# Kernel tuning notes

Hardware: AMD Instinct MI355X
Metric: run time of the kernel (lower is better)

Reference implementation:

```python
import jax, jax.numpy as jnp
import numpy as np

EPS = 1e-6

def feature_map(x):
    # 'elu' feature map: elu(x) + 1 (positive feature map from Katharopoulos et al.)
    return jax.nn.elu(x) + 1.0

def setup_inputs() -> dict:
    key = jax.random.key(0)
    kq, kk, kv = jax.random.split(key, 3)
    B, L, H, D = 4, 2048, 16, 64
    q = jax.random.normal(kq, (B, L, H, D), dtype=jnp.float32)
    k = jax.random.normal(kk, (B, L, H, D), dtype=jnp.float32)
    v = jax.random.normal(kv, (B, L, H, D), dtype=jnp.float32)
    return {"q": q, "k": k, "v": v}

def reference(q, k, v):
    # q, k, v: [N, L, H, D]  (attention_mask=None -> causal linear attention)
    qf = feature_map(q)
    kf = feature_map(k)
    # normalizer: z[n,l,h] = sum_d qf[n,l,h,d] * cumsum_s<=l kf[n,s,h,d]
    z = jnp.einsum('nlhd,nlhd->nlh', qf, jnp.cumsum(kf, axis=1)) + EPS
    # causal_dot_product via scan over sequence with carry S[n,h,d,m]
    B, L, H, D = q.shape
    M = v.shape[-1]
    qs = jnp.moveaxis(qf, 1, 0)  # [L, N, H, D]
    ks = jnp.moveaxis(kf, 1, 0)
    vs = jnp.moveaxis(v, 1, 0)

    def step(S, qkv):
        ql, kl, vl = qkv                              # [N,H,D], [N,H,D], [N,H,M]
        S = S + jnp.einsum('nhd,nhm->nhdm', kl, vl)   # running sum of k v^T
        out = jnp.einsum('nhd,nhdm->nhm', ql, S)
        return S, out

    S0 = jnp.zeros((B, H, D, M), dtype=q.dtype)
    _, outs = jax.lax.scan(step, S0, (qs, ks, vs))    # outs: [L, N, H, M]
    v_ = jnp.moveaxis(outs, 0, 1)                     # [N, L, H, M]
    return v_ / z[..., None]
```

## Files before the change

### kernel.cpp

```cpp
#include <hip/hip_runtime.h>
#include <cstdint>

#define LL 2048
#define HH 16
#define DD 64
#define NC 32
#define LSTR 1024
#define EPSF 1e-6f
#define PAD 72

typedef __bf16 bf16x8 __attribute__((ext_vector_type(8)));
typedef float floatx4 __attribute__((ext_vector_type(4)));
typedef unsigned short ushortx8 __attribute__((ext_vector_type(8)));
typedef unsigned short ushortx4 __attribute__((ext_vector_type(4)));
typedef unsigned short ushortx2 __attribute__((ext_vector_type(2)));

static __device__ __forceinline__ float fmap(float x){ return x > 0.f ? x + 1.f : __expf(x); }
static __device__ __forceinline__ unsigned short f2bf(float f){
    unsigned u = __builtin_bit_cast(unsigned, f);
    u += 0x7fffu + ((u >> 16) & 1u);
    return (unsigned short)(u >> 16);
}
static __device__ __forceinline__ float bf2f(unsigned short s){
    unsigned u = ((unsigned)s) << 16;
    return __builtin_bit_cast(float, u);
}
static __device__ __forceinline__ bf16x8 ldf(const unsigned short* p){
    return __builtin_bit_cast(bf16x8, *(const ushortx8*)p);
}

__global__ __launch_bounds__(256) void k1(const float* __restrict__ kp, const float* __restrict__ vp,
                                          unsigned short* __restrict__ kvt, float* __restrict__ ks)
{
    __shared__ __align__(16) unsigned short kft[DD*PAD];
    __shared__ __align__(16) unsigned short vtt[DD*PAD];
    const int ci = blockIdx.x;
    const int c = ci & 31, bh = ci >> 5, b = bh >> 4, h = bh & 15;
    const int t = threadIdx.x;
    const int64_t gbase = ((int64_t)(b*LL + c*DD)*HH + h)*DD;
#pragma unroll
    for (int i = 0; i < 2; ++i) {
        int flat = t + 256*i;
        int l0 = (flat >> 4) * 2, col = (flat & 15) << 2;
        const float* gk = kp + gbase + (int64_t)l0*LSTR + col;
        const float* gv = vp + gbase + (int64_t)l0*LSTR + col;
        float4 ka = *(const float4*)(gk);
        float4 kb = *(const float4*)(gk + LSTR);
        float4 va = *(const float4*)(gv);
        float4 vb = *(const float4*)(gv + LSTR);
        float kaa[4] = {ka.x,ka.y,ka.z,ka.w}, kbb[4] = {kb.x,kb.y,kb.z,kb.w};
        float vaa[4] = {va.x,va.y,va.z,va.w}, vbb[4] = {vb.x,vb.y,vb.z,vb.w};
#pragma unroll
        for (int e = 0; e < 4; ++e) {
            *(ushortx2*)(kft + (col+e)*PAD + l0) = ushortx2{ f2bf(fmap(kaa[e])), f2bf(fmap(kbb[e])) };
            *(ushortx2*)(vtt + (col+e)*PAD + l0) = ushortx2{ f2bf(vaa[e]), f2bf(vbb[e]) };
        }
    }
    __syncthreads();
    const int w = t >> 6, lane = t & 63, quad = lane >> 4, lr = lane & 15;
    const int m0 = 16*w;
    floatx4 acc[4];
#pragma unroll
    for (int dt = 0; dt < 4; ++dt) acc[dt] = floatx4{0.f,0.f,0.f,0.f};
#pragma unroll
    for (int kk = 0; kk < 2; ++kk) {
        bf16x8 a = ldf(vtt + (m0+lr)*PAD + kk*32 + quad*8);
#pragma unroll
        for (int dt = 0; dt < 4; ++dt) {
            bf16x8 bb = ldf(kft + (dt*16+lr)*PAD + kk*32 + quad*8);
            acc[dt] = __builtin_amdgcn_mfma_f32_16x16x32_bf16(a, bb, acc[dt], 0, 0, 0);
        }
    }
    unsigned short* kvo = kvt + (int64_t)ci*4096;
#pragma unroll
    for (int dt = 0; dt < 4; ++dt)
#pragma unroll
        for (int r = 0; r < 4; ++r)
            kvo[(m0 + quad*4 + r)*DD + dt*16 + lr] = f2bf(acc[dt][r]);
    if (t < DD) {
        float s = 0.f;
#pragma unroll
        for (int j = 0; j < 8; ++j) {
            ushortx8 u = *(const ushortx8*)(kft + t*PAD + j*8);
#pragma unroll
            for (int e = 0; e < 8; ++e) s += bf2f(u[e]);
        }
        ks[(int64_t)ci*DD + t] = s;
    }
}

__global__ __launch_bounds__(256) void k2(unsigned short* __restrict__ kvt, float* __restrict__ ks)
{
    const int blk = blockIdx.x;
    const int bh = blk >> 3, part = blk & 7, t = threadIdx.x;
    unsigned short* base = kvt + (int64_t)bh*NC*4096 + (part*256 + t)*2;
    float r0 = 0.f, r1 = 0.f;
    unsigned x = *(const unsigned*)base;
    for (int c = 0; c < NC-1; ++c) {
        unsigned xn = *(const unsigned*)(base + (int64_t)(c+1)*4096);
        unsigned o = (unsigned)f2bf(r0) | ((unsigned)f2bf(r1) << 16);
        r0 += bf2f((unsigned short)(x & 0xffffu));
        r1 += bf2f((unsigned short)(x >> 16));
        *(unsigned*)(base + (int64_t)c*4096) = o;
        x = xn;
    }
    *(unsigned*)(base + (int64_t)(NC-1)*4096) = (unsigned)f2bf(r0) | ((unsigned)f2bf(r1) << 16);
    if (part == 0 && t < DD) {
        float r = 0.f;
        float* kb = ks + (int64_t)bh*NC*DD + t;
        for (int c = 0; c < NC; ++c) { float xx = kb[(int64_t)c*DD]; kb[(int64_t)c*DD] = r; r += xx; }
    }
}

__global__ __launch_bounds__(256) void k3(const float* __restrict__ qp, const float* __restrict__ kp,
                                          const float* __restrict__ vp,
                                          const unsigned short* __restrict__ kvt,
                                          const float* __restrict__ ks, float* __restrict__ outp)
{
    __shared__ __align__(16) unsigned short qf [DD*PAD];
    __shared__ __align__(16) unsigned short kfx[80*PAD];
    __shared__ __align__(16) unsigned short vtt[DD*PAD];
    __shared__ float zr[DD];
    const int ci = blockIdx.x;
    const int c = ci & 31, bh = ci >> 5, b = bh >> 4, h = bh & 15;
    const int t = threadIdx.x;
    const int64_t gbase = ((int64_t)(b*LL + c*DD)*HH + h)*DD;
    const unsigned short* kvg = kvt + (int64_t)ci*4096;
    const float* ksg = ks + (int64_t)ci*DD;
#pragma unroll
    for (int i = 0; i < 2; ++i) {
        int flat = t + 256*i;
        int l0 = (flat >> 4) * 2, col = (flat & 15) << 2;
        const float* gq = qp + gbase + (int64_t)l0*LSTR + col;
        const float* gk = kp + gbase + (int64_t)l0*LSTR + col;
        const float* gv = vp + gbase + (int64_t)l0*LSTR + col;
        float4 qa = *(const float4*)(gq);
        float4 qb = *(const float4*)(gq + LSTR);
        float4 ka = *(const float4*)(gk);
        float4 kb = *(const float4*)(gk + LSTR);
        float4 va = *(const float4*)(gv);
        float4 vb = *(const float4*)(gv + LSTR);
        *(ushortx4*)(qf + l0*PAD + col)      = ushortx4{ f2bf(fmap(qa.x)), f2bf(fmap(qa.y)), f2bf(fmap(qa.z)), f2bf(fmap(qa.w)) };
        *(ushortx4*)(qf + (l0+1)*PAD + col)  = ushortx4{ f2bf(fmap(qb.x)), f2bf(fmap(qb.y)), f2bf(fmap(qb.z)), f2bf(fmap(qb.w)) };
        *(ushortx4*)(kfx + l0*PAD + col)     = ushortx4{ f2bf(fmap(ka.x)), f2bf(fmap(ka.y)), f2bf(fmap(ka.z)), f2bf(fmap(ka.w)) };
        *(ushortx4*)(kfx + (l0+1)*PAD + col) = ushortx4{ f2bf(fmap(kb.x)), f2bf(fmap(kb.y)), f2bf(fmap(kb.z)), f2bf(fmap(kb.w)) };
        float vaa[4] = {va.x,va.y,va.z,va.w}, vbb[4] = {vb.x,vb.y,vb.z,vb.w};
#pragma unroll
        for (int e = 0; e < 4; ++e)
            *(ushortx2*)(vtt + (col+e)*PAD + l0) = ushortx2{ f2bf(vaa[e]), f2bf(vbb[e]) };
    }
    if (t < 135) *(ushortx8*)(kfx + 65*PAD + t*8) = ushortx8{0,0,0,0,0,0,0,0};
    if (t < DD)  kfx[64*PAD + t] = f2bf(ksg[t]);
    __syncthreads();

    const int w = t >> 6, lane = t & 63, quad = lane >> 4, lr = lane & 15;
    const int l0 = 16*w;
    bf16x8 aq[2];
    aq[0] = ldf(qf + (l0+lr)*PAD + quad*8);
    aq[1] = ldf(qf + (l0+lr)*PAD + 32 + quad*8);
    bf16x8 bs[2][4];
#pragma unroll
    for (int kk = 0; kk < 2; ++kk)
#pragma unroll
        for (int mt = 0; mt < 4; ++mt)
            bs[kk][mt] = ldf(kvg + (mt*16+lr)*DD + kk*32 + quad*8);

    floatx4 sc[5];
#pragma unroll
    for (int tt = 0; tt < 5; ++tt) sc[tt] = floatx4{0.f,0.f,0.f,0.f};
#pragma unroll
    for (int kk = 0; kk < 2; ++kk)
#pragma unroll
        for (int tt = 0; tt < 5; ++tt) {
            bf16x8 bb = ldf(kfx + (tt*16+lr)*PAD + kk*32 + quad*8);
            sc[tt] = __builtin_amdgcn_mfma_f32_16x16x32_bf16(aq[kk], bb, sc[tt], 0, 0, 0);
        }

    float zp[4] = {0.f,0.f,0.f,0.f};
#pragma unroll
    for (int tt = 0; tt < 4; ++tt)
#pragma unroll
        for (int r = 0; r < 4; ++r) {
            int row = l0 + quad*4 + r;
            int col = tt*16 + lr;
            float val = (col <= row) ? sc[tt][r] : 0.f;
            zp[r] += val;
            qf[row*PAD + col] = f2bf(val);
        }
#pragma unroll
    for (int r = 0; r < 4; ++r) zp[r] += (lr == 0) ? sc[4][r] : 0.f;
#pragma unroll
    for (int m = 1; m < 16; m <<= 1)
#pragma unroll
        for (int r = 0; r < 4; ++r) zp[r] += __shfl_xor(zp[r], m, 64);
    if (lr == 0)
#pragma unroll
        for (int r = 0; r < 4; ++r) zr[l0 + quad*4 + r] = 1.f / (zp[r] + EPSF);

    floatx4 oa[4];
#pragma unroll
    for (int mt = 0; mt < 4; ++mt) oa[mt] = floatx4{0.f,0.f,0.f,0.f};
#pragma unroll
    for (int kk = 0; kk < 2; ++kk) {
        bf16x8 a2 = ldf(qf + (l0+lr)*PAD + kk*32 + quad*8);
#pragma unroll
        for (int mt = 0; mt < 4; ++mt) {
            bf16x8 bv = ldf(vtt + (mt*16+lr)*PAD + kk*32 + quad*8);
            oa[mt] = __builtin_amdgcn_mfma_f32_16x16x32_bf16(a2, bv, oa[mt], 0, 0, 0);
        }
    }
#pragma unroll
    for (int kk = 0; kk < 2; ++kk)
#pragma unroll
        for (int mt = 0; mt < 4; ++mt)
            oa[mt] = __builtin_amdgcn_mfma_f32_16x16x32_bf16(aq[kk], bs[kk][mt], oa[mt], 0, 0, 0);
#pragma unroll
    for (int r = 0; r < 4; ++r) {
        int row = l0 + quad*4 + r;
        float rz = zr[row];
#pragma unroll
        for (int mt = 0; mt < 4; ++mt)
            outp[gbase + (int64_t)row*LSTR + mt*16 + lr] = oa[mt][r] * rz;
    }
}

extern "C" void kernel_launch(void* const* d_in, const int* in_sizes, int n_in,
                              void* d_out, int out_size, void* d_ws, size_t ws_size,
                              hipStream_t stream) {
    const float* q = (const float*)d_in[0];
    const float* k = (const float*)d_in[1];
    const float* v = (const float*)d_in[2];
    float* out = (float*)d_out;
    unsigned short* kvt = (unsigned short*)d_ws;
    float* ks = (float*)((char*)d_ws + (size_t)2048*4096*2);
    k1<<<2048, 256, 0, stream>>>(k, v, kvt, ks);
    k2<<<512,  256, 0, stream>>>(kvt, ks);
    k3<<<2048, 256, 0, stream>>>(q, k, v, kvt, ks, out);
}
```

Baseline: 156.0 us.

## Fuse three-kernel chunked linear attention into one sequential-scan kernel with double buffering

```diff
diff --git a/kernel.cpp b/kernel.cpp
--- a/kernel.cpp
+++ b/kernel.cpp
@@ -1,13 +1,8 @@
 #include <hip/hip_runtime.h>
 #include <cstdint>
 
-#define LL 2048
-#define HH 16
-#define DD 64
-#define NC 32
-#define LSTR 1024
 #define EPSF 1e-6f
-#define PAD 72
+#define P 72
 
 typedef __bf16 bf16x8 __attribute__((ext_vector_type(8)));
 typedef float floatx4 __attribute__((ext_vector_type(4)));
@@ -21,206 +16,155 @@
     u += 0x7fffu + ((u >> 16) & 1u);
     return (unsigned short)(u >> 16);
 }
-static __device__ __forceinline__ float bf2f(unsigned short s){
-    unsigned u = ((unsigned)s) << 16;
-    return __builtin_bit_cast(float, u);
-}
 static __device__ __forceinline__ bf16x8 ldf(const unsigned short* p){
     return __builtin_bit_cast(bf16x8, *(const ushortx8*)p);
 }
 
-__global__ __launch_bounds__(256) void k1(const float* __restrict__ kp, const float* __restrict__ vp,
-                                          unsigned short* __restrict__ kvt, float* __restrict__ ks)
+__global__ __launch_bounds__(256, 1) void fused(
+    const float* __restrict__ qp, const float* __restrict__ kp,
+    const float* __restrict__ vp, float* __restrict__ outp)
 {
-    __shared__ __align__(16) unsigned short kft[DD*PAD];
-    __shared__ __align__(16) unsigned short vtt[DD*PAD];
+    __shared__ __align__(16) unsigned short qf [2][64*P];
+    __shared__ __align__(16) unsigned short kf [2][80*P];
+    __shared__ __align__(16) unsigned short kft[2][64*P];
+    __shared__ __align__(16) unsigned short vt [2][16*P];
+    __shared__ __align__(16) unsigned short Sb [2][16*P];
     const int ci = blockIdx.x;
-    const int c = ci & 31, bh = ci >> 5, b = bh >> 4, h = bh & 15;
+    const int bh = ci >> 2, mq = ci & 3;
+    const int b = bh >> 4, h = bh & 15;
     const int t = threadIdx.x;
-    const int64_t gbase = ((int64_t)(b*LL + c*DD)*HH + h)*DD;
+    const int w = t >> 6, lane = t & 63, quad = lane >> 4, lr = lane & 15;
+    const int64_t gbh = ((int64_t)b*2048*16 + (int64_t)h)*64;
+
+    float4 R[9];
+
+    auto issue = [&](int c) {
+        const int64_t g = gbh + (int64_t)c*65536;
 #pragma unroll
-    for (int i = 0; i < 2; ++i) {
-        int flat = t + 256*i;
-        int l0 = (flat >> 4) * 2, col = (flat & 15) << 2;
-        const float* gk = kp + gbase + (int64_t)l0*LSTR + col;
-        const float* gv = vp + gbase + (int64_t)l0*LSTR + col;
-        float4 ka = *(const float4*)(gk);
-        float4 kb = *(const float4*)(gk + LSTR);
-        float4 va = *(const float4*)(gv);
-        float4 vb = *(const float4*)(gv + LSTR);
-        float kaa[4] = {ka.x,ka.y,ka.z,ka.w}, kbb[4] = {kb.x,kb.y,kb.z,kb.w};
-        float vaa[4] = {va.x,va.y,va.z,va.w}, vbb[4] = {vb.x,vb.y,vb.z,vb.w};
+        for (int i = 0; i < 2; ++i) {
+            int flat = t + 256*i, l0 = (flat >> 4)*2, col = (flat & 15)*4;
+            const float* gq = qp + g + (int64_t)l0*1024 + col;
+            const float* gk = kp + g + (int64_t)l0*1024 + col;
+            R[i*2+0] = *(const float4*)(gq);
+            R[i*2+1] = *(const float4*)(gq + 1024);
+            R[4+i*2+0] = *(const float4*)(gk);
+            R[4+i*2+1] = *(const float4*)(gk + 1024);
+        }
+        R[8] = *(const float4*)(vp + g + (int64_t)(t >> 2)*1024 + mq*16 + (t & 3)*4);
+    };
+    auto stage = [&](int buf) {
 #pragma unroll
-        for (int e = 0; e < 4; ++e) {
-            *(ushortx2*)(kft + (col+e)*PAD + l0) = ushortx2{ f2bf(fmap(kaa[e])), f2bf(fmap(kbb[e])) };
-            *(ushortx2*)(vtt + (col+e)*PAD + l0) = ushortx2{ f2bf(vaa[e]), f2bf(vbb[e]) };
+        for (int i = 0; i < 2; ++i) {
+            int flat = t + 256*i, l0 = (flat >> 4)*2, col = (flat & 15)*4;
+            float4 qa = R[i*2+0], qb = R[i*2+1], ka = R[4+i*2+0], kb = R[4+i*2+1];
+            ushortx4 qra = { f2bf(fmap(qa.x)), f2bf(fmap(qa.y)), f2bf(fmap(qa.z)), f2bf(fmap(qa.w)) };
+            ushortx4 qrb = { f2bf(fmap(qb.x)), f2bf(fmap(qb.y)), f2bf(fmap(qb.z)), f2bf(fmap(qb.w)) };
+            ushortx4 kra = { f2bf(fmap(ka.x)), f2bf(fmap(ka.y)), f2bf(fmap(ka.z)), f2bf(fmap(ka.w)) };
+            ushortx4 krb = { f2bf(fmap(kb.x)), f2bf(fmap(kb.y)), f2bf(fmap(kb.z)), f2bf(fmap(kb.w)) };
+            *(ushortx4*)(qf[buf] + l0*P + col)     = qra;
+            *(ushortx4*)(qf[buf] + (l0+1)*P + col) = qrb;
+            *(ushortx4*)(kf[buf] + l0*P + col)     = kra;
+            *(ushortx4*)(kf[buf] + (l0+1)*P + col) = krb;
+#pragma unroll
+            for (int e = 0; e < 4; ++e)
+                *(ushortx2*)(kft[buf] + (col+e)*P + l0) = ushortx2{ kra[e], krb[e] };
         }
+        {
+            int l = t >> 2, m0 = (t & 3)*4;
+            float vv[4] = { R[8].x, R[8].y, R[8].z, R[8].w };
+#pragma unroll
+            for (int e = 0; e < 4; ++e)
+                vt[buf][(m0+e)*P + l] = f2bf(vv[e]);
+        }
+    };
+
+    issue(0);
+    if (t < 144) {
+        ushortx8 z8 = {0,0,0,0,0,0,0,0};
+        *(ushortx8*)(kf[0] + 64*P + t*8) = z8;
+        *(ushortx8*)(kf[1] + 64*P + t*8) = z8;
+        *(ushortx8*)(Sb[0] + t*8) = z8;
     }
+    stage(0);
     __syncthreads();
-    const int w = t >> 6, lane = t & 63, quad = lane >> 4, lr = lane & 15;
-    const int m0 = 16*w;
-    floatx4 acc[4];
+
+    floatx4 accS = {0.f,0.f,0.f,0.f};
+    float kpr = 0.f;
+    const ushortx8 ou = {0x3F80,0x3F80,0x3F80,0x3F80,0x3F80,0x3F80,0x3F80,0x3F80};
+    const bf16x8 ones = __builtin_bit_cast(bf16x8, ou);
+    const int l0 = 16*w;
+
+#pragma unroll 1
+    for (int c = 0; c < 32; ++c) {
+        const int cur = c & 1, nxt = cur ^ 1;
+        if (c < 31) issue(c+1);
+
+        bf16x8 aq0 = ldf(qf[cur] + (l0+lr)*P + quad*8);
+        bf16x8 aq1 = ldf(qf[cur] + (l0+lr)*P + 32 + quad*8);
+        floatx4 sc[5];
 #pragma unroll
-    for (int dt = 0; dt < 4; ++dt) acc[dt] = floatx4{0.f,0.f,0.f,0.f};
+        for (int tt = 0; tt < 5; ++tt) sc[tt] = floatx4{0.f,0.f,0.f,0.f};
 #pragma unroll
-    for (int kk = 0; kk < 2; ++kk) {
-        bf16x8 a = ldf(vtt + (m0+lr)*PAD + kk*32 + quad*8);
+        for (int tt = 0; tt < 5; ++tt) {
+            bf16x8 b0 = ldf(kf[cur] + (tt*16+lr)*P + quad*8);
+            bf16x8 b1 = ldf(kf[cur] + (tt*16+lr)*P + 32 + quad*8);
+            sc[tt] = __builtin_amdgcn_mfma_f32_16x16x32_bf16(aq0, b0, sc[tt], 0, 0, 0);
+            sc[tt] = __builtin_amdgcn_mfma_f32_16x16x32_bf16(aq1, b1, sc[tt], 0, 0, 0);
+        }
+        float zp[4] = {0.f,0.f,0.f,0.f};
 #pragma unroll
-        for (int dt = 0; dt < 4; ++dt) {
-            bf16x8 bb = ldf(kft + (dt*16+lr)*PAD + kk*32 + quad*8);
-            acc[dt] = __builtin_amdgcn_mfma_f32_16x16x32_bf16(a, bb, acc[dt], 0, 0, 0);
+        for (int tt = 0; tt < 4; ++tt)
+#pragma unroll
+            for (int r = 0; r < 4; ++r) {
+                int row = l0 + quad*4 + r, col = tt*16 + lr;
+                float val = (col <= row) ? sc[tt][r] : 0.f;
+                zp[r] += val;
+                qf[cur][row*P + col] = f2bf(val);
+            }
+#pragma unroll
+        for (int r = 0; r < 4; ++r) zp[r] += (lr == 0) ? sc[4][r] : 0.f;
+#pragma unroll
+        for (int m = 1; m < 16; m <<= 1)
+#pragma unroll
+            for (int r = 0; r < 4; ++r) zp[r] += __shfl_xor(zp[r], m, 64);
+        float rz[4];
+#pragma unroll
+        for (int r = 0; r < 4; ++r) rz[r] = 1.f / (zp[r] + EPSF);
+
+        bf16x8 a20 = ldf(qf[cur] + (l0+lr)*P + quad*8);
+        bf16x8 a21 = ldf(qf[cur] + (l0+lr)*P + 32 + quad*8);
+        bf16x8 bv0 = ldf(vt[cur] + lr*P + quad*8);
+        bf16x8 bv1 = ldf(vt[cur] + lr*P + 32 + quad*8);
+        bf16x8 bS0 = ldf(Sb[cur] + lr*P + quad*8);
+        bf16x8 bS1 = ldf(Sb[cur] + lr*P + 32 + quad*8);
+        floatx4 oa = {0.f,0.f,0.f,0.f};
+        oa = __builtin_amdgcn_mfma_f32_16x16x32_bf16(a20, bv0, oa, 0, 0, 0);
+        oa = __builtin_amdgcn_mfma_f32_16x16x32_bf16(a21, bv1, oa, 0, 0, 0);
+        oa = __builtin_amdgcn_mfma_f32_16x16x32_bf16(aq0, bS0, oa, 0, 0, 0);
+        oa = __builtin_amdgcn_mfma_f32_16x16x32_bf16(aq1, bS1, oa, 0, 0, 0);
+        {
+            const int64_t go = gbh + (int64_t)c*65536 + mq*16 + lr;
+#pragma unroll
+            for (int r = 0; r < 4; ++r)
+                outp[go + (int64_t)(l0 + quad*4 + r)*1024] = oa[r] * rz[r];
         }
-    }
-    unsigned short* kvo = kvt + (int64_t)ci*4096;
-#pragma unroll
-    for (int dt = 0; dt < 4; ++dt)
+
+        bf16x8 t0 = ldf(kft[cur] + (l0+lr)*P + quad*8);
+        bf16x8 t1 = ldf(kft[cur] + (l0+lr)*P + 32 + quad*8);
+        accS = __builtin_amdgcn_mfma_f32_16x16x32_bf16(t0, bv0, accS, 0, 0, 0);
+        accS = __builtin_amdgcn_mfma_f32_16x16x32_bf16(t1, bv1, accS, 0, 0, 0);
 #pragma unroll
         for (int r = 0; r < 4; ++r)
-            kvo[(m0 + quad*4 + r)*DD + dt*16 + lr] = f2bf(acc[dt][r]);
-    if (t < DD) {
-        float s = 0.f;
-#pragma unroll
-        for (int j = 0; j < 8; ++j) {
-            ushortx8 u = *(const ushortx8*)(kft + t*PAD + j*8);
-#pragma unroll
-            for (int e = 0; e < 8; ++e) s += bf2f(u[e]);
-        }
-        ks[(int64_t)ci*DD + t] = s;
-    }
-}
+            Sb[nxt][lr*P + l0 + quad*4 + r] = f2bf(accS[r]);
 
-__global__ __launch_bounds__(256) void k2(unsigned short* __restrict__ kvt, float* __restrict__ ks)
-{
-    const int blk = blockIdx.x;
-    const int bh = blk >> 3, part = blk & 7, t = threadIdx.x;
-    unsigned short* base = kvt + (int64_t)bh*NC*4096 + (part*256 + t)*2;
-    float r0 = 0.f, r1 = 0.f;
-    unsigned x = *(const unsigned*)base;
-    for (int c = 0; c < NC-1; ++c) {
-        unsigned xn = *(const unsigned*)(base + (int64_t)(c+1)*4096);
-        unsigned o = (unsigned)f2bf(r0) | ((unsigned)f2bf(r1) << 16);
-        r0 += bf2f((unsigned short)(x & 0xffffu));
-        r1 += bf2f((unsigned short)(x >> 16));
-        *(unsigned*)(base + (int64_t)c*4096) = o;
-        x = xn;
-    }
-    *(unsigned*)(base + (int64_t)(NC-1)*4096) = (unsigned)f2bf(r0) | ((unsigned)f2bf(r1) << 16);
-    if (part == 0 && t < DD) {
-        float r = 0.f;
-        float* kb = ks + (int64_t)bh*NC*DD + t;
-        for (int c = 0; c < NC; ++c) { float xx = kb[(int64_t)c*DD]; kb[(int64_t)c*DD] = r; r += xx; }
-    }
-}
+        floatx4 colc = {0.f,0.f,0.f,0.f};
+        colc = __builtin_amdgcn_mfma_f32_16x16x32_bf16(ones, t0, colc, 0, 0, 0);
+        colc = __builtin_amdgcn_mfma_f32_16x16x32_bf16(ones, t1, colc, 0, 0, 0);
+        kpr += colc[0];
+        if (quad == 0) kf[nxt][64*P + l0 + lr] = f2bf(kpr);
 
-__global__ __launch_bounds__(256) void k3(const float* __restrict__ qp, const float* __restrict__ kp,
-                                          const float* __restrict__ vp,
-                                          const unsigned short* __restrict__ kvt,
-                                          const float* __restrict__ ks, float* __restrict__ outp)
-{
-    __shared__ __align__(16) unsigned short qf [DD*PAD];
-    __shared__ __align__(16) unsigned short kfx[80*PAD];
-    __shared__ __align__(16) unsigned short vtt[DD*PAD];
-    __shared__ float zr[DD];
-    const int ci = blockIdx.x;
-    const int c = ci & 31, bh = ci >> 5, b = bh >> 4, h = bh & 15;
-    const int t = threadIdx.x;
-    const int64_t gbase = ((int64_t)(b*LL + c*DD)*HH + h)*DD;
-    const unsigned short* kvg = kvt + (int64_t)ci*4096;
-    const float* ksg = ks + (int64_t)ci*DD;
-#pragma unroll
-    for (int i = 0; i < 2; ++i) {
-        int flat = t + 256*i;
-        int l0 = (flat >> 4) * 2, col = (flat & 15) << 2;
-        const float* gq = qp + gbase + (int64_t)l0*LSTR + col;
-        const float* gk = kp + gbase + (int64_t)l0*LSTR + col;
-        const float* gv = vp + gbase + (int64_t)l0*LSTR + col;
-        float4 qa = *(const float4*)(gq);
-        float4 qb = *(const float4*)(gq + LSTR);
-        float4 ka = *(const float4*)(gk);
-        float4 kb = *(const float4*)(gk + LSTR);
-        float4 va = *(const float4*)(gv);
-        float4 vb = *(const float4*)(gv + LSTR);
-        *(ushortx4*)(qf + l0*PAD + col)      = ushortx4{ f2bf(fmap(qa.x)), f2bf(fmap(qa.y)), f2bf(fmap(qa.z)), f2bf(fmap(qa.w)) };
-        *(ushortx4*)(qf + (l0+1)*PAD + col)  = ushortx4{ f2bf(fmap(qb.x)), f2bf(fmap(qb.y)), f2bf(fmap(qb.z)), f2bf(fmap(qb.w)) };
-        *(ushortx4*)(kfx + l0*PAD + col)     = ushortx4{ f2bf(fmap(ka.x)), f2bf(fmap(ka.y)), f2bf(fmap(ka.z)), f2bf(fmap(ka.w)) };
-        *(ushortx4*)(kfx + (l0+1)*PAD + col) = ushortx4{ f2bf(fmap(kb.x)), f2bf(fmap(kb.y)), f2bf(fmap(kb.z)), f2bf(fmap(kb.w)) };
-        float vaa[4] = {va.x,va.y,va.z,va.w}, vbb[4] = {vb.x,vb.y,vb.z,vb.w};
-#pragma unroll
-        for (int e = 0; e < 4; ++e)
-            *(ushortx2*)(vtt + (col+e)*PAD + l0) = ushortx2{ f2bf(vaa[e]), f2bf(vbb[e]) };
-    }
-    if (t < 135) *(ushortx8*)(kfx + 65*PAD + t*8) = ushortx8{0,0,0,0,0,0,0,0};
-    if (t < DD)  kfx[64*PAD + t] = f2bf(ksg[t]);
-    __syncthreads();
-
-    const int w = t >> 6, lane = t & 63, quad = lane >> 4, lr = lane & 15;
-    const int l0 = 16*w;
-    bf16x8 aq[2];
-    aq[0] = ldf(qf + (l0+lr)*PAD + quad*8);
-    aq[1] = ldf(qf + (l0+lr)*PAD + 32 + quad*8);
-    bf16x8 bs[2][4];
-#pragma unroll
-    for (int kk = 0; kk < 2; ++kk)
-#pragma unroll
-        for (int mt = 0; mt < 4; ++mt)
-            bs[kk][mt] = ldf(kvg + (mt*16+lr)*DD + kk*32 + quad*8);
-
-    floatx4 sc[5];
-#pragma unroll
-    for (int tt = 0; tt < 5; ++tt) sc[tt] = floatx4{0.f,0.f,0.f,0.f};
-#pragma unroll
-    for (int kk = 0; kk < 2; ++kk)
-#pragma unroll
-        for (int tt = 0; tt < 5; ++tt) {
-            bf16x8 bb = ldf(kfx + (tt*16+lr)*PAD + kk*32 + quad*8);
-            sc[tt] = __builtin_amdgcn_mfma_f32_16x16x32_bf16(aq[kk], bb, sc[tt], 0, 0, 0);
-        }
-
-    float zp[4] = {0.f,0.f,0.f,0.f};
-#pragma unroll
-    for (int tt = 0; tt < 4; ++tt)
-#pragma unroll
-        for (int r = 0; r < 4; ++r) {
-            int row = l0 + quad*4 + r;
-            int col = tt*16 + lr;
-            float val = (col <= row) ? sc[tt][r] : 0.f;
-            zp[r] += val;
-            qf[row*PAD + col] = f2bf(val);
-        }
-#pragma unroll
-    for (int r = 0; r < 4; ++r) zp[r] += (lr == 0) ? sc[4][r] : 0.f;
-#pragma unroll
-    for (int m = 1; m < 16; m <<= 1)
-#pragma unroll
-        for (int r = 0; r < 4; ++r) zp[r] += __shfl_xor(zp[r], m, 64);
-    if (lr == 0)
-#pragma unroll
-        for (int r = 0; r < 4; ++r) zr[l0 + quad*4 + r] = 1.f / (zp[r] + EPSF);
-
-    floatx4 oa[4];
-#pragma unroll
-    for (int mt = 0; mt < 4; ++mt) oa[mt] = floatx4{0.f,0.f,0.f,0.f};
-#pragma unroll
-    for (int kk = 0; kk < 2; ++kk) {
-        bf16x8 a2 = ldf(qf + (l0+lr)*PAD + kk*32 + quad*8);
-#pragma unroll
-        for (int mt = 0; mt < 4; ++mt) {
-            bf16x8 bv = ldf(vtt + (mt*16+lr)*PAD + kk*32 + quad*8);
-            oa[mt] = __builtin_amdgcn_mfma_f32_16x16x32_bf16(a2, bv, oa[mt], 0, 0, 0);
-        }
-    }
-#pragma unroll
-    for (int kk = 0; kk < 2; ++kk)
-#pragma unroll
-        for (int mt = 0; mt < 4; ++mt)
-            oa[mt] = __builtin_amdgcn_mfma_f32_16x16x32_bf16(aq[kk], bs[kk][mt], oa[mt], 0, 0, 0);
-#pragma unroll
-    for (int r = 0; r < 4; ++r) {
-        int row = l0 + quad*4 + r;
-        float rz = zr[row];
-#pragma unroll
-        for (int mt = 0; mt < 4; ++mt)
-            outp[gbase + (int64_t)row*LSTR + mt*16 + lr] = oa[mt][r] * rz;
+        if (c < 31) stage(nxt);
+        __syncthreads();
     }
 }
 
@@ -231,9 +175,5 @@
     const float* k = (const float*)d_in[1];
     const float* v = (const float*)d_in[2];
     float* out = (float*)d_out;
-    unsigned short* kvt = (unsigned short*)d_ws;
-    float* ks = (float*)((char*)d_ws + (size_t)2048*4096*2);
-    k1<<<2048, 256, 0, stream>>>(k, v, kvt, ks);
-    k2<<<512,  256, 0, stream>>>(kvt, ks);
-    k3<<<2048, 256, 0, stream>>>(q, k, v, kvt, ks, out);
+    fused<<<256, 256, 0, stream>>>(q, k, v, out);
 }
```

Result: slower. 178.5 us (+14.4%).
